# Kernel tuning notes

Hardware: AMD Instinct MI355X
Metric: run time of the kernel (lower is better)

The kernel has to match this reference:

```python
import jax, jax.numpy as jnp
import numpy as np

# --- config (matches init_kwargs) ---
NUM_EXPERTS = 8
TOP_K = 2
GROUP_DET = 1024
GROUP_CLS = 512
D_MODEL = 768
MLP_DIM = 3072


def setup_inputs() -> dict:
    key = jax.random.key(0)
    ks = jax.random.split(key, 8)
    scale = 0.02
    return {
        "x_det": jax.random.normal(ks[0], (16, 1024, D_MODEL), dtype=jnp.float32),
        "x_cls": jax.random.normal(ks[1], (16, 256, D_MODEL), dtype=jnp.float32),
        "w_router_det": jax.random.normal(ks[2], (D_MODEL, NUM_EXPERTS), dtype=jnp.float32) * scale,
        "w_router_cls": jax.random.normal(ks[3], (D_MODEL, NUM_EXPERTS), dtype=jnp.float32) * scale,
        "w1": jax.random.normal(ks[4], (NUM_EXPERTS, D_MODEL, MLP_DIM), dtype=jnp.float32) * scale,
        "b1": jnp.zeros((NUM_EXPERTS, MLP_DIM), dtype=jnp.float32),
        "w2": jax.random.normal(ks[5], (NUM_EXPERTS, MLP_DIM, D_MODEL), dtype=jnp.float32) * scale,
        "b2": jnp.zeros((NUM_EXPERTS, D_MODEL), dtype=jnp.float32),
    }


def _route(xg, w_router, top_k, num_experts, capacity):
    """Top-k per-item routing with expert capacity (vmoe-style einsum dispatcher).

    xg: [G, S, D] grouped tokens. Returns dispatch [G,S,E,C], combine [G,S,E,C].
    """
    G, S, _ = xg.shape
    gates = jax.nn.softmax(jnp.einsum("gsd,de->gse", xg, w_router))  # [G,S,E]
    gval, gidx = jax.lax.top_k(gates, top_k)  # [G,S,k]
    # k-major ordering: slot-0 choices of all tokens get capacity priority.
    mask = jax.nn.one_hot(gidx, num_experts, dtype=xg.dtype)  # [G,S,k,E]
    mask = mask.transpose(0, 2, 1, 3).reshape(G, top_k * S, num_experts)
    pos = jnp.cumsum(mask, axis=1) - 1.0  # position within expert buffer
    keep = mask * (pos < capacity)
    disp = keep[..., None] * jax.nn.one_hot(pos, capacity, dtype=xg.dtype)  # [G,kS,E,C]
    disp = disp.reshape(G, top_k, S, num_experts, capacity)
    combine = jnp.einsum("gksec,gks->gsec", disp, gval.transpose(0, 2, 1))
    dispatch = disp.sum(axis=1)  # [G,S,E,C] (one-hot: a token goes to each expert <=1 time)
    return dispatch, combine


def _expert_mlp(expert_in, w1, b1, w2, b2):
    # expert_in: [E, N, D] -> vmapped-expert MLP (grouped GEMM)
    h = jax.nn.gelu(jnp.einsum("end,edh->enh", expert_in, w1) + b1[:, None, :])
    return jnp.einsum("enh,ehd->end", h, w2) + b2[:, None, :]


def _moe(x, w_router, w1, b1, w2, b2, group_size):
    B, S, D = x.shape
    G = (B * S) // group_size
    capacity = (TOP_K * group_size) // NUM_EXPERTS
    xg = x.reshape(G, group_size, D)
    dispatch, combine = _route(xg, w_router, TOP_K, NUM_EXPERTS, capacity)
    expert_in = jnp.einsum("gsec,gsd->egcd", dispatch, xg)  # [E,G,C,D]
    E, _, C, _ = expert_in.shape
    y = _expert_mlp(expert_in.reshape(E, G * C, D), w1, b1, w2, b2).reshape(E, G, C, D)
    out = jnp.einsum("gsec,egcd->gsd", combine, y)
    return out.reshape(B, S, D)


def reference(x_det, x_cls, w_router_det, w_router_cls, w1, b1, w2, b2):
    out_det = _moe(x_det, w_router_det, w1, b1, w2, b2, GROUP_DET)
    out_cls = _moe(x_cls, w_router_cls, w1, b1, w2, b2, GROUP_CLS)
    # concatenate the two streams along the sequence axis for a single output
    return jnp.concatenate([out_det, out_cls], axis=1)
```

## Files before the change

### kernel.cpp

```cpp
#include <hip/hip_runtime.h>
#include <cstdint>
#include <cstddef>

#define NE 8
#define DMODEL 768
#define MLPDIM 3072
#define NDET 16384
#define NCLS 4096
#define NTOK 20480
#define ROWS_PER_E 5120
#define TOT_ROWS 40960

typedef float f32x4 __attribute__((ext_vector_type(4)));
typedef __bf16 bf16x8 __attribute__((ext_vector_type(8)));

__device__ __forceinline__ unsigned short f2bf(float f) {
    unsigned u = __float_as_uint(f);
    u += 0x7FFFu + ((u >> 16) & 1u);
    return (unsigned short)(u >> 16);
}
__device__ __forceinline__ float bf2f(unsigned v) {
    return __uint_as_float(v << 16);
}
__device__ __forceinline__ float gelu_f(float x) {
    float u = 0.7978845608028654f * (x + 0.044715f * x * x * x);
    float t = __expf(-2.0f * fabsf(u));
    float th = __builtin_copysignf((1.0f - t) * __frcp_rn(1.0f + t), u);
    return 0.5f * x * (1.0f + th);
}

__device__ __forceinline__ void gload16(const void* g, void* l) {
    __builtin_amdgcn_global_load_lds(
        (const __attribute__((address_space(1))) unsigned int*)g,
        (__attribute__((address_space(3))) unsigned int*)l, 16, 0, 0);
}

__global__ void k_router(const float* __restrict__ xd, const float* __restrict__ xc,
                         const float* __restrict__ wrd, const float* __restrict__ wrc,
                         ushort* __restrict__ xbf,
                         int* __restrict__ e1, int* __restrict__ e2,
                         float* __restrict__ g1, float* __restrict__ g2) {
    int wave = threadIdx.x >> 6, lane = threadIdx.x & 63;
    int t = blockIdx.x * 4 + wave;
    if (t >= NTOK) return;
    const float* xrow;
    const float* w;
    if (t < NDET) { xrow = xd + (size_t)t * DMODEL; w = wrd; }
    else          { xrow = xc + (size_t)(t - NDET) * DMODEL; w = wrc; }
    ushort* xbrow = xbf + (size_t)t * DMODEL;
    float acc[8];
    #pragma unroll
    for (int e = 0; e < 8; e++) acc[e] = 0.0f;
    #pragma unroll
    for (int kk = 0; kk < DMODEL / 64; kk++) {
        int k = kk * 64 + lane;
        float xv = xrow[k];
        xbrow[k] = f2bf(xv);
        const float* wr = w + k * 8;
        #pragma unroll
        for (int e = 0; e < 8; e++) acc[e] += xv * wr[e];
    }
    #pragma unroll
    for (int e = 0; e < 8; e++) {
        #pragma unroll
        for (int off = 32; off > 0; off >>= 1) acc[e] += __shfl_xor(acc[e], off);
    }
    int i1 = 0; float v1 = acc[0];
    #pragma unroll
    for (int e = 1; e < 8; e++) if (acc[e] > v1) { v1 = acc[e]; i1 = e; }
    int i2 = -1; float v2 = -1e30f;
    #pragma unroll
    for (int e = 0; e < 8; e++) if (e != i1 && acc[e] > v2) { v2 = acc[e]; i2 = e; }
    float Z = 0.0f;
    #pragma unroll
    for (int e = 0; e < 8; e++) Z += __expf(acc[e] - v1);
    if (lane == 0) {
        e1[t] = i1; e2[t] = i2;
        g1[t] = 1.0f / Z;
        g2[t] = __expf(v2 - v1) / Z;
    }
}

__global__ void k_transpose_bf(const float* __restrict__ in, ushort* __restrict__ out,
                               int K, int N) {
    __shared__ float tile[32][33];
    int e = blockIdx.z;
    const float* A = in + (size_t)e * K * N;
    ushort* B = out + (size_t)e * N * K;
    int n0 = blockIdx.x * 32, k0 = blockIdx.y * 32;
    int tx = threadIdx.x, ty = threadIdx.y;
    float4 v = *(const float4*)(A + (size_t)(k0 + ty) * N + n0 + tx * 4);
    tile[ty][tx * 4 + 0] = v.x; tile[ty][tx * 4 + 1] = v.y;
    tile[ty][tx * 4 + 2] = v.z; tile[ty][tx * 4 + 3] = v.w;
    __syncthreads();
    ushort4 o;
    o.x = f2bf(tile[tx * 4 + 0][ty]);
    o.y = f2bf(tile[tx * 4 + 1][ty]);
    o.z = f2bf(tile[tx * 4 + 2][ty]);
    o.w = f2bf(tile[tx * 4 + 3][ty]);
    *(ushort4*)(B + (size_t)(n0 + ty) * K + k0 + tx * 4) = o;
}

__global__ void k_scan(const int* __restrict__ e1, const int* __restrict__ e2,
                       int* __restrict__ slot_map, int* __restrict__ r1, int* __restrict__ r2) {
    int g = blockIdx.x;
    int lane = threadIdx.x;
    int S, C, base;
    if (g < 16) { S = 1024; C = 256; base = g * 1024; }
    else        { S = 512;  C = 128; base = NDET + (g - 16) * 512; }
    int cnt[8];
    #pragma unroll
    for (int e = 0; e < 8; e++) cnt[e] = 0;
    unsigned long long lower = (lane == 0) ? 0ULL : ((~0ULL) >> (64 - lane));
    int nch = (2 * S) >> 6;
    for (int ch = 0; ch < nch; ch++) {
        int n = ch * 64 + lane;
        int k = (n >= S) ? 1 : 0;
        int s = n - k * S;
        int tok = base + s;
        int e = k ? e2[tok] : e1[tok];
        int pos = 0;
        #pragma unroll
        for (int ee = 0; ee < 8; ee++) {
            unsigned long long m = __ballot(e == ee);
            if (e == ee) pos = cnt[ee] + __popcll(m & lower);
            cnt[ee] += __popcll(m);
        }
        int r = -1;
        if (pos < C) {
            int local = (g < 16) ? (g * 256 + pos) : (4096 + (g - 16) * 128 + pos);
            r = e * ROWS_PER_E + local;
            slot_map[r] = tok;
        }
        if (k == 0) r1[tok] = r; else r2[tok] = r;
    }
}

template<int KTOT, int NTOT, int MODE>
__global__ __launch_bounds__(512, 4) void k_gemm(
    const ushort* __restrict__ Asrc, const int* __restrict__ slot_map,
    const ushort* __restrict__ wtBase, const float* __restrict__ biasBase,
    ushort* __restrict__ Cdst, int eBase) {
    constexpr int KSTEPS = KTOT / 64;
    constexpr int NBN = NTOT / 128;
    __shared__ __align__(1024) ushort As[128 * 64];
    __shared__ __align__(1024) ushort Bs[128 * 64];

    const int q = gridDim.x >> 3;
    const int id2 = (blockIdx.x & 7) * q + (blockIdx.x >> 3);
    const int mb = id2 / NBN, nb = id2 - mb * NBN;
    const int e = eBase + mb / (ROWS_PER_E / 128);
    const int m0 = mb * 128;
    const int rbase = eBase * ROWS_PER_E + m0;
    const int n0 = nb * 128;
    const ushort* Bt = wtBase + (size_t)e * KTOT * NTOT;
    const float* bias = biasBase + (size_t)e * NTOT;

    const int t = threadIdx.x, lane = t & 63, wave = t >> 6;
    const int g8 = lane >> 3;
    const int p8 = lane & 7;
    const int swz = ((p8 ^ g8) << 4);

    const char* aS[2];
    const char* bS[2];
    #pragma unroll
    for (int j = 0; j < 2; j++) {
        int r = wave * 16 + j * 8 + g8;
        size_t arow;
        if (MODE == 0) { int tk = slot_map[rbase + r]; arow = (size_t)(tk < 0 ? 0 : tk); }
        else           { arow = (size_t)(m0 + r); }
        aS[j] = (const char*)(Asrc + arow * KTOT) + swz;
        bS[j] = (const char*)(Bt + (size_t)(n0 + r) * KTOT) + swz;
    }

    auto ISSUE = [&](int ks) {
        int o = ks * 128;
        #pragma unroll
        for (int j = 0; j < 2; j++) {
            gload16(aS[j] + o, As + (wave * 16 + j * 8) * 64);
            gload16(bS[j] + o, Bs + (wave * 16 + j * 8) * 64);
        }
    };

    const int wr = wave >> 2, wc = wave & 3;
    const int arow = wr * 64 + (lane & 15);
    const int brow = wc * 32 + (lane & 15);
    const int kq = lane >> 4, l7 = lane & 7;
    const int ch0 = ((kq) ^ l7) << 3;
    const int ch1 = ((4 + kq) ^ l7) << 3;

    f32x4 acc[4][2] = {};
    ISSUE(0);
    for (int ks = 0; ks < KSTEPS; ks++) {
        __syncthreads();
        bf16x8 a0[4], b0[2], a1[4], b1[2];
        #pragma unroll
        for (int mt = 0; mt < 4; mt++)
            a0[mt] = *(const bf16x8*)(As + (arow + mt * 16) * 64 + ch0);
        #pragma unroll
        for (int nt = 0; nt < 2; nt++)
            b0[nt] = *(const bf16x8*)(Bs + (brow + nt * 16) * 64 + ch0);
        #pragma unroll
        for (int mt = 0; mt < 4; mt++)
            a1[mt] = *(const bf16x8*)(As + (arow + mt * 16) * 64 + ch1);
        #pragma unroll
        for (int nt = 0; nt < 2; nt++)
            b1[nt] = *(const bf16x8*)(Bs + (brow + nt * 16) * 64 + ch1);
        __syncthreads();
        if (ks + 1 < KSTEPS) ISSUE(ks + 1);
        #pragma unroll
        for (int mt = 0; mt < 4; mt++) {
            #pragma unroll
            for (int nt = 0; nt < 2; nt++)
                acc[mt][nt] = __builtin_amdgcn_mfma_f32_16x16x32_bf16(a0[mt], b0[nt], acc[mt][nt], 0, 0, 0);
        }
        #pragma unroll
        for (int mt = 0; mt < 4; mt++) {
            #pragma unroll
            for (int nt = 0; nt < 2; nt++)
                acc[mt][nt] = __builtin_amdgcn_mfma_f32_16x16x32_bf16(a1[mt], b1[nt], acc[mt][nt], 0, 0, 0);
        }
    }

    const int ccol = wc * 32 + (lane & 15);
    float bv[2];
    #pragma unroll
    for (int nt = 0; nt < 2; nt++) bv[nt] = bias[n0 + ccol + nt * 16];

    if (MODE == 0) {
        #pragma unroll
        for (int mt = 0; mt < 4; mt++) {
            #pragma unroll
            for (int j = 0; j < 4; j++) {
                int row = m0 + wr * 64 + mt * 16 + (lane >> 4) * 4 + j;
                #pragma unroll
                for (int nt = 0; nt < 2; nt++) {
                    float v = gelu_f(acc[mt][nt][j] + bv[nt]);
                    Cdst[(size_t)row * NTOT + n0 + ccol + nt * 16] = f2bf(v);
                }
            }
        }
    } else {
        #pragma unroll
        for (int mt = 0; mt < 4; mt++) {
            #pragma unroll
            for (int j = 0; j < 4; j++) {
                int grow = rbase + wr * 64 + mt * 16 + (lane >> 4) * 4 + j;
                #pragma unroll
                for (int nt = 0; nt < 2; nt++) {
                    float v = acc[mt][nt][j] + bv[nt];
                    Cdst[(size_t)grow * NTOT + n0 + ccol + nt * 16] = f2bf(v);
                }
            }
        }
    }
}

__global__ void k_combine(const ushort* __restrict__ y,
                          const int* __restrict__ r1, const int* __restrict__ r2,
                          const float* __restrict__ g1, const float* __restrict__ g2,
                          float* __restrict__ out) {
    int t = blockIdx.x;
    int d = threadIdx.x;
    int a = r1[t], b = r2[t];
    float wa = g1[t], wb = g2[t];
    size_t opos;
    if (t < NDET) { int bb = t >> 10, s = t & 1023; opos = ((size_t)bb * 1280 + s) * 768; }
    else { int tt = t - NDET; int bb = tt >> 8, s = tt & 255; opos = ((size_t)bb * 1280 + 1024 + s) * 768; }
    int di = d * 4;
    float4 o = make_float4(0.f, 0.f, 0.f, 0.f);
    if (a >= 0) {
        uint2 v = *(const uint2*)(y + (size_t)a * 768 + di);
        o.x += wa * bf2f(v.x & 0xffffu); o.y += wa * bf2f(v.x >> 16);
        o.z += wa * bf2f(v.y & 0xffffu); o.w += wa * bf2f(v.y >> 16);
    }
    if (b >= 0) {
        uint2 v = *(const uint2*)(y + (size_t)b * 768 + di);
        o.x += wb * bf2f(v.x & 0xffffu); o.y += wb * bf2f(v.x >> 16);
        o.z += wb * bf2f(v.y & 0xffffu); o.w += wb * bf2f(v.y >> 16);
    }
    *(float4*)(out + opos + di) = o;
}

extern "C" void kernel_launch(void* const* d_in, const int* in_sizes, int n_in,
                              void* d_out, int out_size, void* d_ws, size_t ws_size,
                              hipStream_t stream) {
    const float* xd  = (const float*)d_in[0];
    const float* xc  = (const float*)d_in[1];
    const float* wrd = (const float*)d_in[2];
    const float* wrc = (const float*)d_in[3];
    const float* w1  = (const float*)d_in[4];
    const float* b1  = (const float*)d_in[5];
    const float* w2  = (const float*)d_in[6];
    const float* b2  = (const float*)d_in[7];
    float* out = (float*)d_out;

    size_t off = 0;
    char* base = (char*)d_ws;
    auto alloc = [&](size_t bytes) -> char* {
        char* r = base + off;
        off += (bytes + 255) & ~(size_t)255;
        return r;
    };
    ushort* xbf = (ushort*)alloc((size_t)NTOK * DMODEL * 2);
    ushort* w1t = (ushort*)alloc((size_t)NE * MLPDIM * DMODEL * 2);
    ushort* w2t = (ushort*)alloc((size_t)NE * DMODEL * MLPDIM * 2);
    ushort* y   = (ushort*)alloc((size_t)TOT_ROWS * DMODEL * 2);
    int*   slot_map = (int*)alloc((size_t)TOT_ROWS * 4);
    int*   e1 = (int*)alloc((size_t)NTOK * 4);
    int*   e2 = (int*)alloc((size_t)NTOK * 4);
    float* g1 = (float*)alloc((size_t)NTOK * 4);
    float* g2 = (float*)alloc((size_t)NTOK * 4);
    int*   r1 = (int*)alloc((size_t)NTOK * 4);
    int*   r2 = (int*)alloc((size_t)NTOK * 4);

    const size_t h_per_e = (size_t)ROWS_PER_E * MLPDIM * 2;
    int chunkE = 0;
    for (int c = NE; c >= 2; c >>= 1)
        if (off + c * h_per_e <= ws_size) { chunkE = c; break; }
    if (!chunkE) return;
    ushort* h = (ushort*)alloc((size_t)chunkE * h_per_e);

    hipMemsetAsync(slot_map, 0xFF, (size_t)TOT_ROWS * 4, stream);

    k_router<<<NTOK / 4, 256, 0, stream>>>(xd, xc, wrd, wrc, xbf, e1, e2, g1, g2);
    k_transpose_bf<<<dim3(MLPDIM / 32, DMODEL / 32, NE), dim3(8, 32), 0, stream>>>(w1, w1t, DMODEL, MLPDIM);
    k_transpose_bf<<<dim3(DMODEL / 32, MLPDIM / 32, NE), dim3(8, 32), 0, stream>>>(w2, w2t, MLPDIM, DMODEL);
    k_scan<<<24, 64, 0, stream>>>(e1, e2, slot_map, r1, r2);

    for (int e0 = 0; e0 < NE; e0 += chunkE) {
        int nmb = chunkE * (ROWS_PER_E / 128);
        k_gemm<DMODEL, MLPDIM, 0><<<nmb * (MLPDIM / 128), 512, 0, stream>>>(
            xbf, slot_map, w1t, b1, h, e0);
        k_gemm<MLPDIM, DMODEL, 1><<<nmb * (DMODEL / 128), 512, 0, stream>>>(
            h, slot_map, w2t, b2, y, e0);
    }

    k_combine<<<NTOK, 192, 0, stream>>>(y, r1, r2, g1, g2, out);
}
```

Measured before the change: 645.3 us.

## Enlarge GEMM tiles to 256x256 with double-buffered LDS and MFMA priority

The grouped expert GEMM moves from a 128x128 tile to a 256x256 tile. Each wave now computes 128x64 with 8x4 MFMA fragments. LDS becomes double-buffered, so the next K-tile load is issued right after a single barrier, and s_setprio raises wave priority around the MFMA burst. This cuts global-memory traffic per FLOP and removes one barrier per step, at the cost of 128KB of LDS, more registers (launch bounds relaxed to 2) and fewer blocks in the grid.

```diff
diff --git a/kernel.cpp b/kernel.cpp
--- a/kernel.cpp
+++ b/kernel.cpp
@@ -137,22 +137,22 @@
 }
 
 template<int KTOT, int NTOT, int MODE>
-__global__ __launch_bounds__(512, 4) void k_gemm(
+__global__ __launch_bounds__(512, 2) void k_gemm(
     const ushort* __restrict__ Asrc, const int* __restrict__ slot_map,
     const ushort* __restrict__ wtBase, const float* __restrict__ biasBase,
     ushort* __restrict__ Cdst, int eBase) {
-    constexpr int KSTEPS = KTOT / 64;
-    constexpr int NBN = NTOT / 128;
-    __shared__ __align__(1024) ushort As[128 * 64];
-    __shared__ __align__(1024) ushort Bs[128 * 64];
+    constexpr int KT = KTOT / 64;
+    constexpr int NBN = NTOT / 256;
+    __shared__ __align__(1024) ushort As[2][256 * 64];
+    __shared__ __align__(1024) ushort Bs[2][256 * 64];
 
     const int q = gridDim.x >> 3;
     const int id2 = (blockIdx.x & 7) * q + (blockIdx.x >> 3);
     const int mb = id2 / NBN, nb = id2 - mb * NBN;
-    const int e = eBase + mb / (ROWS_PER_E / 128);
-    const int m0 = mb * 128;
+    const int e = eBase + mb / (ROWS_PER_E / 256);
+    const int m0 = mb * 256;
     const int rbase = eBase * ROWS_PER_E + m0;
-    const int n0 = nb * 128;
+    const int n0 = nb * 256;
     const ushort* Bt = wtBase + (size_t)e * KTOT * NTOT;
     const float* bias = biasBase + (size_t)e * NTOT;
 
@@ -161,11 +161,11 @@
     const int p8 = lane & 7;
     const int swz = ((p8 ^ g8) << 4);
 
-    const char* aS[2];
-    const char* bS[2];
-    #pragma unroll
-    for (int j = 0; j < 2; j++) {
-        int r = wave * 16 + j * 8 + g8;
+    const char* aS[4];
+    const char* bS[4];
+    #pragma unroll
+    for (int j = 0; j < 4; j++) {
+        int r = wave * 32 + j * 8 + g8;
         size_t arow;
         if (MODE == 0) { int tk = slot_map[rbase + r]; arow = (size_t)(tk < 0 ? 0 : tk); }
         else           { arow = (size_t)(m0 + r); }
@@ -173,84 +173,62 @@
         bS[j] = (const char*)(Bt + (size_t)(n0 + r) * KTOT) + swz;
     }
 
-    auto ISSUE = [&](int ks) {
-        int o = ks * 128;
-        #pragma unroll
-        for (int j = 0; j < 2; j++) {
-            gload16(aS[j] + o, As + (wave * 16 + j * 8) * 64);
-            gload16(bS[j] + o, Bs + (wave * 16 + j * 8) * 64);
+    auto ISSUE = [&](int kt, int buf) {
+        size_t o = (size_t)kt * 128;
+        #pragma unroll
+        for (int j = 0; j < 4; j++) {
+            gload16(aS[j] + o, &As[buf][(wave * 32 + j * 8) * 64]);
+            gload16(bS[j] + o, &Bs[buf][(wave * 32 + j * 8) * 64]);
         }
     };
 
     const int wr = wave >> 2, wc = wave & 3;
-    const int arow = wr * 64 + (lane & 15);
-    const int brow = wc * 32 + (lane & 15);
-    const int kq = lane >> 4, l7 = lane & 7;
-    const int ch0 = ((kq) ^ l7) << 3;
-    const int ch1 = ((4 + kq) ^ l7) << 3;
-
-    f32x4 acc[4][2] = {};
-    ISSUE(0);
-    for (int ks = 0; ks < KSTEPS; ks++) {
+    const int l15 = lane & 15, kq = lane >> 4, l7 = lane & 7;
+
+    f32x4 acc[8][4] = {};
+    ISSUE(0, 0);
+    int cur = 0;
+    for (int kt = 0; kt < KT; ++kt) {
         __syncthreads();
-        bf16x8 a0[4], b0[2], a1[4], b1[2];
-        #pragma unroll
-        for (int mt = 0; mt < 4; mt++)
-            a0[mt] = *(const bf16x8*)(As + (arow + mt * 16) * 64 + ch0);
-        #pragma unroll
-        for (int nt = 0; nt < 2; nt++)
-            b0[nt] = *(const bf16x8*)(Bs + (brow + nt * 16) * 64 + ch0);
-        #pragma unroll
-        for (int mt = 0; mt < 4; mt++)
-            a1[mt] = *(const bf16x8*)(As + (arow + mt * 16) * 64 + ch1);
-        #pragma unroll
-        for (int nt = 0; nt < 2; nt++)
-            b1[nt] = *(const bf16x8*)(Bs + (brow + nt * 16) * 64 + ch1);
-        __syncthreads();
-        if (ks + 1 < KSTEPS) ISSUE(ks + 1);
-        #pragma unroll
-        for (int mt = 0; mt < 4; mt++) {
+        if (kt + 1 < KT) ISSUE(kt + 1, cur ^ 1);
+        #pragma unroll
+        for (int kc = 0; kc < 2; kc++) {
+            const int ch = ((kq + 4 * kc) ^ l7) << 3;
+            bf16x8 af[8], bfr[4];
             #pragma unroll
-            for (int nt = 0; nt < 2; nt++)
-                acc[mt][nt] = __builtin_amdgcn_mfma_f32_16x16x32_bf16(a0[mt], b0[nt], acc[mt][nt], 0, 0, 0);
-        }
-        #pragma unroll
-        for (int mt = 0; mt < 4; mt++) {
+            for (int mf = 0; mf < 8; mf++)
+                af[mf] = *(const bf16x8*)(&As[cur][(wr * 128 + mf * 16 + l15) * 64 + ch]);
             #pragma unroll
-            for (int nt = 0; nt < 2; nt++)
-                acc[mt][nt] = __builtin_amdgcn_mfma_f32_16x16x32_bf16(a1[mt], b1[nt], acc[mt][nt], 0, 0, 0);
-        }
-    }
-
-    const int ccol = wc * 32 + (lane & 15);
-    float bv[2];
-    #pragma unroll
-    for (int nt = 0; nt < 2; nt++) bv[nt] = bias[n0 + ccol + nt * 16];
-
-    if (MODE == 0) {
-        #pragma unroll
-        for (int mt = 0; mt < 4; mt++) {
+            for (int nf = 0; nf < 4; nf++)
+                bfr[nf] = *(const bf16x8*)(&Bs[cur][(wc * 64 + nf * 16 + l15) * 64 + ch]);
+            __builtin_amdgcn_s_setprio(1);
             #pragma unroll
-            for (int j = 0; j < 4; j++) {
-                int row = m0 + wr * 64 + mt * 16 + (lane >> 4) * 4 + j;
+            for (int mf = 0; mf < 8; mf++) {
                 #pragma unroll
-                for (int nt = 0; nt < 2; nt++) {
-                    float v = gelu_f(acc[mt][nt][j] + bv[nt]);
-                    Cdst[(size_t)row * NTOT + n0 + ccol + nt * 16] = f2bf(v);
-                }
+                for (int nf = 0; nf < 4; nf++)
+                    acc[mf][nf] = __builtin_amdgcn_mfma_f32_16x16x32_bf16(af[mf], bfr[nf], acc[mf][nf], 0, 0, 0);
             }
-        }
-    } else {
-        #pragma unroll
-        for (int mt = 0; mt < 4; mt++) {
+            __builtin_amdgcn_s_setprio(0);
+        }
+        cur ^= 1;
+    }
+
+    const int ccolb = n0 + wc * 64 + l15;
+    float bv[4];
+    #pragma unroll
+    for (int nf = 0; nf < 4; nf++) bv[nf] = bias[ccolb + nf * 16];
+
+    const int rowb = (MODE == 0 ? m0 : rbase) + wr * 128 + (lane >> 4) * 4;
+    #pragma unroll
+    for (int mf = 0; mf < 8; mf++) {
+        #pragma unroll
+        for (int j = 0; j < 4; j++) {
+            size_t roff = (size_t)(rowb + mf * 16 + j) * NTOT;
             #pragma unroll
-            for (int j = 0; j < 4; j++) {
-                int grow = rbase + wr * 64 + mt * 16 + (lane >> 4) * 4 + j;
-                #pragma unroll
-                for (int nt = 0; nt < 2; nt++) {
-                    float v = acc[mt][nt][j] + bv[nt];
-                    Cdst[(size_t)grow * NTOT + n0 + ccol + nt * 16] = f2bf(v);
-                }
+            for (int nf = 0; nf < 4; nf++) {
+                float v = acc[mf][nf][j] + bv[nf];
+                if (MODE == 0) v = gelu_f(v);
+                Cdst[roff + ccolb + nf * 16] = f2bf(v);
             }
         }
     }
@@ -329,10 +307,10 @@
     k_scan<<<24, 64, 0, stream>>>(e1, e2, slot_map, r1, r2);
 
     for (int e0 = 0; e0 < NE; e0 += chunkE) {
-        int nmb = chunkE * (ROWS_PER_E / 128);
-        k_gemm<DMODEL, MLPDIM, 0><<<nmb * (MLPDIM / 128), 512, 0, stream>>>(
+        int nmb = chunkE * (ROWS_PER_E / 256);
+        k_gemm<DMODEL, MLPDIM, 0><<<nmb * (MLPDIM / 256), 512, 0, stream>>>(
             xbf, slot_map, w1t, b1, h, e0);
-        k_gemm<MLPDIM, DMODEL, 1><<<nmb * (DMODEL / 128), 512, 0, stream>>>(
+        k_gemm<MLPDIM, DMODEL, 1><<<nmb * (DMODEL / 256), 512, 0, stream>>>(
             h, slot_map, w2t, b2, y, e0);
     }
 
```

Result: slower. 675.1 us (+4.6%).

## Double-buffer LDS tiles in expert GEMM with one barrier per K-step

Applied to the files above, without the earlier changes.

Replaces the single LDS buffer, which needed two barriers per K-step, with ping-pong A/B buffers. The next tile is prefetched into the alternate buffer while MFMAs consume the current one, and there is one waitcnt plus barrier per step. It also raises wave priority around the MFMA block. The goal is to hide global-load latency and cut synchronisation. In exchange LDS use doubles to 64KB per block, which may reduce occupancy against the launch bound of 4 blocks per CU.

```diff
diff --git a/kernel.cpp b/kernel.cpp
--- a/kernel.cpp
+++ b/kernel.cpp
@@ -141,10 +141,12 @@
     const ushort* __restrict__ Asrc, const int* __restrict__ slot_map,
     const ushort* __restrict__ wtBase, const float* __restrict__ biasBase,
     ushort* __restrict__ Cdst, int eBase) {
-    constexpr int KSTEPS = KTOT / 64;
+    constexpr int KT = KTOT / 64;
     constexpr int NBN = NTOT / 128;
-    __shared__ __align__(1024) ushort As[128 * 64];
-    __shared__ __align__(1024) ushort Bs[128 * 64];
+    __shared__ __align__(1024) ushort As0[128 * 64];
+    __shared__ __align__(1024) ushort As1[128 * 64];
+    __shared__ __align__(1024) ushort Bs0[128 * 64];
+    __shared__ __align__(1024) ushort Bs1[128 * 64];
 
     const int q = gridDim.x >> 3;
     const int id2 = (blockIdx.x & 7) * q + (blockIdx.x >> 3);
@@ -173,83 +175,86 @@
         bS[j] = (const char*)(Bt + (size_t)(n0 + r) * KTOT) + swz;
     }
 
-    auto ISSUE = [&](int ks) {
-        int o = ks * 128;
+    auto STAGE = [&](int kt, ushort* WA, ushort* WB) {
+        size_t o = (size_t)kt * 128;
         #pragma unroll
         for (int j = 0; j < 2; j++) {
-            gload16(aS[j] + o, As + (wave * 16 + j * 8) * 64);
-            gload16(bS[j] + o, Bs + (wave * 16 + j * 8) * 64);
+            gload16(aS[j] + o, WA + (wave * 16 + j * 8) * 64);
+            gload16(bS[j] + o, WB + (wave * 16 + j * 8) * 64);
         }
     };
 
     const int wr = wave >> 2, wc = wave & 3;
-    const int arow = wr * 64 + (lane & 15);
-    const int brow = wc * 32 + (lane & 15);
-    const int kq = lane >> 4, l7 = lane & 7;
-    const int ch0 = ((kq) ^ l7) << 3;
-    const int ch1 = ((4 + kq) ^ l7) << 3;
+    const int l15 = lane & 15, kq = lane >> 4, l7 = lane & 7;
+    const int ch[2] = { ((kq) ^ l7) << 3, ((4 + kq) ^ l7) << 3 };
 
     f32x4 acc[4][2] = {};
-    ISSUE(0);
-    for (int ks = 0; ks < KSTEPS; ks++) {
-        __syncthreads();
-        bf16x8 a0[4], b0[2], a1[4], b1[2];
-        #pragma unroll
-        for (int mt = 0; mt < 4; mt++)
-            a0[mt] = *(const bf16x8*)(As + (arow + mt * 16) * 64 + ch0);
-        #pragma unroll
-        for (int nt = 0; nt < 2; nt++)
-            b0[nt] = *(const bf16x8*)(Bs + (brow + nt * 16) * 64 + ch0);
-        #pragma unroll
-        for (int mt = 0; mt < 4; mt++)
-            a1[mt] = *(const bf16x8*)(As + (arow + mt * 16) * 64 + ch1);
-        #pragma unroll
-        for (int nt = 0; nt < 2; nt++)
-            b1[nt] = *(const bf16x8*)(Bs + (brow + nt * 16) * 64 + ch1);
-        __syncthreads();
-        if (ks + 1 < KSTEPS) ISSUE(ks + 1);
-        #pragma unroll
-        for (int mt = 0; mt < 4; mt++) {
-            #pragma unroll
-            for (int nt = 0; nt < 2; nt++)
-                acc[mt][nt] = __builtin_amdgcn_mfma_f32_16x16x32_bf16(a0[mt], b0[nt], acc[mt][nt], 0, 0, 0);
-        }
-        #pragma unroll
-        for (int mt = 0; mt < 4; mt++) {
-            #pragma unroll
-            for (int nt = 0; nt < 2; nt++)
-                acc[mt][nt] = __builtin_amdgcn_mfma_f32_16x16x32_bf16(a1[mt], b1[nt], acc[mt][nt], 0, 0, 0);
-        }
-    }
-
-    const int ccol = wc * 32 + (lane & 15);
+
+    auto BODY = [&](int kt, const ushort* RA, const ushort* RB, ushort* WA, ushort* WB) {
+        const bool last = (kt + 1 >= KT);
+        if (!last) STAGE(kt + 1, WA, WB);
+        #pragma unroll
+        for (int kc = 0; kc < 2; kc++) {
+            bf16x8 af[4], bfr[2];
+            #pragma unroll
+            for (int mi = 0; mi < 4; mi++)
+                af[mi] = *(const bf16x8*)(&RA[(wr * 64 + mi * 16 + l15) * 64 + ch[kc]]);
+            #pragma unroll
+            for (int nf = 0; nf < 2; nf++)
+                bfr[nf] = *(const bf16x8*)(&RB[(wc * 32 + nf * 16 + l15) * 64 + ch[kc]]);
+            __builtin_amdgcn_s_setprio(1);
+            #pragma unroll
+            for (int mi = 0; mi < 4; mi++) {
+                #pragma unroll
+                for (int nf = 0; nf < 2; nf++)
+                    acc[mi][nf] = __builtin_amdgcn_mfma_f32_16x16x32_bf16(
+                        af[mi], bfr[nf], acc[mi][nf], 0, 0, 0);
+            }
+            __builtin_amdgcn_s_setprio(0);
+        }
+        if (!last) {
+            asm volatile("s_waitcnt vmcnt(0)" ::: "memory");
+            __builtin_amdgcn_s_barrier();
+        }
+    };
+
+    STAGE(0, As0, Bs0);
+    asm volatile("s_waitcnt vmcnt(0)" ::: "memory");
+    __builtin_amdgcn_s_barrier();
+
+    for (int kt = 0; kt < KT; kt += 2) {
+        BODY(kt,     As0, Bs0, As1, Bs1);
+        BODY(kt + 1, As1, Bs1, As0, Bs0);
+    }
+
+    const int ccol = wc * 32 + l15;
     float bv[2];
     #pragma unroll
-    for (int nt = 0; nt < 2; nt++) bv[nt] = bias[n0 + ccol + nt * 16];
+    for (int nf = 0; nf < 2; nf++) bv[nf] = bias[n0 + ccol + nf * 16];
 
     if (MODE == 0) {
         #pragma unroll
-        for (int mt = 0; mt < 4; mt++) {
+        for (int mi = 0; mi < 4; mi++) {
             #pragma unroll
             for (int j = 0; j < 4; j++) {
-                int row = m0 + wr * 64 + mt * 16 + (lane >> 4) * 4 + j;
+                int row = m0 + wr * 64 + mi * 16 + (lane >> 4) * 4 + j;
                 #pragma unroll
-                for (int nt = 0; nt < 2; nt++) {
-                    float v = gelu_f(acc[mt][nt][j] + bv[nt]);
-                    Cdst[(size_t)row * NTOT + n0 + ccol + nt * 16] = f2bf(v);
+                for (int nf = 0; nf < 2; nf++) {
+                    float v = gelu_f(acc[mi][nf][j] + bv[nf]);
+                    Cdst[(size_t)row * NTOT + n0 + ccol + nf * 16] = f2bf(v);
                 }
             }
         }
     } else {
         #pragma unroll
-        for (int mt = 0; mt < 4; mt++) {
+        for (int mi = 0; mi < 4; mi++) {
             #pragma unroll
             for (int j = 0; j < 4; j++) {
-                int grow = rbase + wr * 64 + mt * 16 + (lane >> 4) * 4 + j;
+                int grow = rbase + wr * 64 + mi * 16 + (lane >> 4) * 4 + j;
                 #pragma unroll
-                for (int nt = 0; nt < 2; nt++) {
-                    float v = acc[mt][nt][j] + bv[nt];
-                    Cdst[(size_t)grow * NTOT + n0 + ccol + nt * 16] = f2bf(v);
+                for (int nf = 0; nf < 2; nf++) {
+                    float v = acc[mi][nf][j] + bv[nf];
+                    Cdst[(size_t)grow * NTOT + n0 + ccol + nf * 16] = f2bf(v);
                 }
             }
         }
```

Measured after the change: 648.3 us. Within noise of the previous version (+0.5%).
